# Performance work log

Hardware: AMD Instinct MI355X
Metric: run time of the kernel (lower is better)

Reference implementation:

```python
import jax, jax.numpy as jnp
import numpy as np

B, N = 2, 1024
DIM = 1024
DQK = 128
NUM_KEYS = 256
NUM_MEM = NUM_KEYS * NUM_KEYS
TOPK = 32
RANK = 2
HEADS = 2
DV = 512
KCONV = 5
MARGIN = 0.15
AUX_W = 0.1
MEM_LR = 10.0
RMS_EPS = 1.1920929e-07  # torch.finfo(float32).eps (RMSNorm eps=None default)
LN_EPS = 1e-5


def setup_inputs() -> dict:
    key = jax.random.key(0)
    ks = jax.random.split(key, 6)
    return {
        "tokens": jax.random.normal(ks[0], (B, N, DIM), jnp.float32),
        "rms_w": jnp.ones((DIM,), jnp.float32),
        "conv_w": jax.random.normal(ks[1], (DIM, 1, KCONV), jnp.float32) * 0.1,
        "conv_b": jnp.zeros((DIM,), jnp.float32),
        "wq": jax.random.normal(ks[2], (DQK, DIM), jnp.float32) * 0.02,
        "qln_w": jnp.ones((DQK,), jnp.float32),
        "keys": jax.random.normal(ks[3], (2, RANK, NUM_KEYS, DQK), jnp.float32) * 0.01,
        "core": jax.random.normal(ks[4], (HEADS, RANK, RANK), jnp.float32) * 0.01,
        "memories": jax.random.normal(ks[5], (NUM_MEM, DV), jnp.float32) * 0.01,
    }


def _forward(tokens, rms_w, conv_w, conv_b, wq, qln_w, keys, core, memories):
    # prenorm RMSNorm
    x = tokens * jax.lax.rsqrt(jnp.mean(tokens * tokens, -1, keepdims=True) + RMS_EPS) * rms_w
    # SVD of core; rank-1 merge vectors (first left/right singular vectors)
    u, s, vh = jnp.linalg.svd(core, full_matrices=False)
    u_vec = u[..., :, 0]   # (H, R)
    t_vec = vh[..., 0, :]  # (H, R)  == v[..., :, 0]
    aux = jnp.sum(jnp.mean(jnp.square(jax.nn.relu(s[:, 1:] - MARGIN)), -1)) * AUX_W
    # causal depthwise conv (left-pad KCONV-1)
    xc = jnp.swapaxes(x, 1, 2)  # (B, D, N)
    xc = jax.lax.conv_general_dilated(
        xc, conv_w, (1,), [(KCONV - 1, 0)],
        feature_group_count=DIM, dimension_numbers=('NCH', 'OIH', 'NCH'))
    x = jnp.swapaxes(xc + conv_b[None, :, None], 1, 2)
    # queries + LayerNorm (no bias). NOTE: original applies key_ln but then uses
    # the raw self.keys in the einsum, so key normalization is a no-op; replicated.
    q = x @ wq.T
    mu = jnp.mean(q, -1, keepdims=True)
    var = jnp.mean(jnp.square(q - mu), -1, keepdims=True)
    q = (q - mu) * jax.lax.rsqrt(var + LN_EPS) * qln_w
    # product-key scores: (2, B, N, M, R)
    sc = jnp.einsum('bnd,crmd->cbnmr', q, keys)
    row_sc, col_sc = sc[0], sc[1]  # (B, N, M, R)
    m_row = jnp.einsum('bnmr,hr->hbnm', row_sc, u_vec)
    m_col = jnp.einsum('bnmr,hr->hbnm', col_sc, t_vec)
    _, top_row = jax.lax.top_k(m_row, TOPK)  # (H, B, N, K)
    _, top_col = jax.lax.top_k(m_col, TOPK)
    # candidate flat memory indices: outer sum -> (H, B, N, K*K)
    idx = (top_row * NUM_KEYS)[..., :, None] + top_col[..., None, :]
    idx = idx.reshape(HEADS, B, N, TOPK * TOPK)
    # gather per-rank scores at the top row/col keys
    rs = jnp.broadcast_to(row_sc[None], (HEADS,) + row_sc.shape)
    cs = jnp.broadcast_to(col_sc[None], (HEADS,) + col_sc.shape)
    ri = jnp.broadcast_to(top_row[..., None], top_row.shape + (RANK,))
    ci = jnp.broadcast_to(top_col[..., None], top_col.shape + (RANK,))
    f_row = jnp.take_along_axis(rs, ri, axis=3)  # (H, B, N, K, R)
    f_col = jnp.take_along_axis(cs, ci, axis=3)
    # bilinear core combine over ranks -> (H, B, N, K, K)
    scores = jnp.einsum('hbnir,hbnjs,hrs->hbnij', f_row, f_col, core)
    scores = scores.reshape(HEADS, B, N, TOPK * TOPK)
    fs, top_m = jax.lax.top_k(scores, TOPK)
    f_idx = jnp.take_along_axis(idx, top_m, axis=-1)  # (H, B, N, K)
    fs = jax.nn.sigmoid(fs)
    # gather from memory table: (H, B, N, K, DV)
    mem = memories[f_idx]
    # scale_gradient exactly as written: detach(t) - s*t + detach(s*t)  (grad = -s)
    scaled = mem * MEM_LR
    mem = jax.lax.stop_gradient(mem) - scaled + jax.lax.stop_gradient(scaled)
    agg = jnp.einsum('hbnkd,hbnk->hbnd', mem, fs)
    out = jnp.transpose(agg, (1, 2, 0, 3)).reshape(B, N, HEADS * DV)
    # combine_values_to_out is Identity (heads * dim_values == dim)
    return out, aux


def reference(tokens, rms_w, conv_w, conv_b, wq, qln_w, keys, core, memories):
    return _forward(tokens, rms_w, conv_w, conv_b, wq, qln_w, keys, core, memories)
```

## Files before the change

kernel.cpp:

```cpp
#include <hip/hip_runtime.h>
#include <math.h>


#define ROWS 2048

__device__ inline double dsgn(double x, double y) { return (y >= 0.0) ? fabs(x) : -fabs(x); }

__device__ void dlasv2_dev(double f, double g, double h,
                           double& ssmin, double& ssmax,
                           double& snr, double& csr, double& snl, double& csl)
{
  const double EPSD = 2.2204460492503131e-16;
  double ft = f, fa = fabs(f), ht = h, ha = fabs(h);
  int pmax = 1;
  bool swp = (ha > fa);
  if (swp) { pmax = 3; double tp = ft; ft = ht; ht = tp; tp = fa; fa = ha; ha = tp; }
  double gt = g, ga = fabs(gt);
  double clt = 0.0, crt = 0.0, slt = 0.0, srt = 0.0;
  if (ga == 0.0) {
    ssmin = ha; ssmax = fa; clt = 1.0; crt = 1.0; slt = 0.0; srt = 0.0;
  } else {
    bool gasmal = true;
    if (ga > fa) {
      pmax = 2;
// ... 45 lines not shown
  for (int hh = 0; hh < 2; hh++) {
    double a = (double)core[hh * 4 + 0];
    double b = (double)core[hh * 4 + 1];
    double c = (double)core[hh * 4 + 2];
    double d = (double)core[hh * 4 + 3];
    double tau = 0.0, v2 = 0.0, d1, e, d2;
    if (c != 0.0) {
      double nrm  = sqrt(a * a + c * c);
      double beta = (a >= 0.0) ? -nrm : nrm;
      tau = (beta - a) / beta;
      v2  = c / (a - beta);
      double wsum = b + v2 * d;
      d1 = beta;
      e  = b - tau * wsum;
      d2 = d - tau * v2 * wsum;
    } else { d1 = a; e = b; d2 = d; }
    double ssmin, ssmax, snr, csr, snl, csl;
    dlasv2_dev(d1, e, d2, ssmin, ssmax, snr, csr, snl, csl);
    double t0 = csl + v2 * snl;
    double u0 = csl - tau * t0;
    double u1 = snl - tau * v2 * t0;
    double sg = (ssmax < 0.0) ? -1.0 : 1.0;
    misc[hh * 2 + 0]     = (float)u0;
    misc[hh * 2 + 1]     = (float)u1;
    misc[4 + hh * 2 + 0] = (float)(sg * csr);
    misc[4 + hh * 2 + 1] = (float)(sg * snr);
    double s2 = fabs(ssmin);
    double rl = s2 - 0.15; if (rl < 0.0) rl = 0.0;
    aux += rl * rl;
  }
  aux_out[0] = (float)(aux * 0.1);
}

__global__ __launch_bounds__(256) void conv_kernel(const float* __restrict__ tokens,
                                                   const float* __restrict__ rms_w,
                                                   const float* __restrict__ conv_w,
                                                   const float* __restrict__ conv_b,
                                                   const float* __restrict__ core,
                                                   float* __restrict__ misc,
                                                   float* __restrict__ aux_out,
                                                   float* __restrict__ x2)
{
  __shared__ float x_l[12][1024];
  __shared__ float red[12][4];
  __shared__ float inv_s[12];
  const int t    = threadIdx.x;
  const int row0 = blockIdx.x * 8;
  const int n0   = row0 & 1023;
  const int c0   = t * 4;

  float sq[12];
  #pragma unroll
  for (int s = 0; s < 12; s++) {
    float4 v = make_float4(0.f, 0.f, 0.f, 0.f);
    if (n0 - 4 + s >= 0)
      v = *(const float4*)(tokens + (size_t)(row0 - 4 + s) * 1024 + c0);
    *(float4*)&x_l[s][c0] = v;
    sq[s] = v.x * v.x + v.y * v.y + v.z * v.z + v.w * v.w;
  }
  #pragma unroll
  for (int off = 32; off; off >>= 1) {
    #pragma unroll
    for (int s = 0; s < 12; s++) sq[s] += __shfl_down(sq[s], off, 64);
  }
  const int lane = t & 63, wv_id = t >> 6;
  if (lane == 0) {
    #pragma unroll
    for (int s = 0; s < 12; s++) red[s][wv_id] = sq[s];
  }
  __syncthreads();
  if (t < 12)
    inv_s[t] = rsqrtf((red[t][0] + red[t][1] + red[t][2] + red[t][3]) * (1.0f / 1024.0f)
                      + 1.1920929e-07f);
  __syncthreads();
  #pragma unroll
  for (int s = 0; s < 12; s++) {
    float iv = inv_s[s];
    float4 v = *(float4*)&x_l[s][c0];
    v.x *= iv; v.y *= iv; v.z *= iv; v.w *= iv;
    *(float4*)&x_l[s][c0] = v;
  }
  float wv[20];
  const float* cw = conv_w + (size_t)c0 * 5;
  #pragma unroll
  for (int i = 0; i < 5; i++) {
    float4 u = *(const float4*)(cw + i * 4);
    wv[i * 4 + 0] = u.x; wv[i * 4 + 1] = u.y; wv[i * 4 + 2] = u.z; wv[i * 4 + 3] = u.w;
  }
  float4 rw = *(const float4*)(rms_w + c0);
  float4 cb = *(const float4*)(conv_b + c0);
  #pragma unroll
  for (int r = 0; r < 8; r++) {
    float4 acc = make_float4(0.f, 0.f, 0.f, 0.f);
    #pragma unroll
    for (int k = 0; k < 5; k++) {
      float4 x4 = *(const float4*)&x_l[r + k][c0];
      acc.x = fmaf(x4.x, wv[0 * 5 + k], acc.x);
      acc.y = fmaf(x4.y, wv[1 * 5 + k], acc.y);
      acc.z = fmaf(x4.z, wv[2 * 5 + k], acc.z);
      acc.w = fmaf(x4.w, wv[3 * 5 + k], acc.w);
    }
    acc.x = acc.x * rw.x + cb.x;
    acc.y = acc.y * rw.y + cb.y;
    acc.z = acc.z * rw.z + cb.z;
    acc.w = acc.w * rw.w + cb.w;
    *(float4*)(x2 + (size_t)(row0 + r) * 1024 + c0) = acc;
  }
  if (blockIdx.x == 0 && t == 0) do_svd(core, misc, aux_out);
}

__global__ __launch_bounds__(256) void gemm_kernel(const float* __restrict__ A, int lda,
                                                   const float* __restrict__ Bm, int ldb,
                                                   float* __restrict__ C, int ldc,
                                                   int koffy, int coffy, int poffy)
{
  __shared__ __align__(16) float a_lds[32 * 64];
  __shared__ __align__(16) float b_lds[32 * 128];
  const int t  = threadIdx.x;
  const int rb = blockIdx.x * 64;
  const int kb = blockIdx.y * koffy;
  const int cb = blockIdx.y * coffy;
  C += (size_t)blockIdx.y * (size_t)poffy;
  const int tx = t & 31, ty = t >> 5;
  const int c0 = tx * 4, r0 = ty * 8;
  float acc[8][4];
  #pragma unroll
  for (int i = 0; i < 8; i++)
    #pragma unroll
    for (int j = 0; j < 4; j++) acc[i][j] = 0.0f;

  const int ra = t & 63,  kqa = (t >> 6) * 8;
  const int ob = t >> 1,  kqb = (t & 1) * 16;

  for (int kt = 0; kt < 4; kt++) {
    const int k0 = kb + kt * 32;
    {
      const float* ap = A + (size_t)(rb + ra) * lda + k0 + kqa;
      float4 a0 = *(const float4*)(ap);
      float4 a1 = *(const float4*)(ap + 4);
      a_lds[(kqa + 0) * 64 + ra] = a0.x;
      a_lds[(kqa + 1) * 64 + ra] = a0.y;
      a_lds[(kqa + 2) * 64 + ra] = a0.z;
      a_lds[(kqa + 3) * 64 + ra] = a0.w;
      a_lds[(kqa + 4) * 64 + ra] = a1.x;
      a_lds[(kqa + 5) * 64 + ra] = a1.y;
      a_lds[(kqa + 6) * 64 + ra] = a1.z;
      a_lds[(kqa + 7) * 64 + ra] = a1.w;
    }
    {
      const float* bp = Bm + (size_t)(cb + ob) * ldb + k0 + kqb;
      float4 b0 = *(const float4*)(bp);
      float4 b1 = *(const float4*)(bp + 4);
      float4 b2 = *(const float4*)(bp + 8);
      float4 b3 = *(const float4*)(bp + 12);
      b_lds[(kqb +  0) * 128 + ob] = b0.x;
      b_lds[(kqb +  1) * 128 + ob] = b0.y;
      b_lds[(kqb +  2) * 128 + ob] = b0.z;
      b_lds[(kqb +  3) * 128 + ob] = b0.w;
      b_lds[(kqb +  4) * 128 + ob] = b1.x;
      b_lds[(kqb +  5) * 128 + ob] = b1.y;
      b_lds[(kqb +  6) * 128 + ob] = b1.z;
      b_lds[(kqb +  7) * 128 + ob] = b1.w;
      b_lds[(kqb +  8) * 128 + ob] = b2.x;
      b_lds[(kqb +  9) * 128 + ob] = b2.y;
      b_lds[(kqb + 10) * 128 + ob] = b2.z;
      b_lds[(kqb + 11) * 128 + ob] = b2.w;
      b_lds[(kqb + 12) * 128 + ob] = b3.x;
      b_lds[(kqb + 13) * 128 + ob] = b3.y;
      b_lds[(kqb + 14) * 128 + ob] = b3.z;
      b_lds[(kqb + 15) * 128 + ob] = b3.w;
    }
    __syncthreads();
    #pragma unroll
    for (int k = 0; k < 32; k++) {
      float4 av0 = *(const float4*)(a_lds + k * 64 + r0);
      float4 av1 = *(const float4*)(a_lds + k * 64 + r0 + 4);
      float4 bv  = *(const float4*)(b_lds + k * 128 + c0);
      float ar[8] = {av0.x, av0.y, av0.z, av0.w, av1.x, av1.y, av1.z, av1.w};
      float br[4] = {bv.x, bv.y, bv.z, bv.w};
      #pragma unroll
      for (int i = 0; i < 8; i++)
        #pragma unroll
        for (int j = 0; j < 4; j++)
          acc[i][j] = fmaf(ar[i], br[j], acc[i][j]);
    }
    __syncthreads();
  }
  #pragma unroll
  for (int i = 0; i < 8; i++) {
    float4 o4; o4.x = acc[i][0]; o4.y = acc[i][1]; o4.z = acc[i][2]; o4.w = acc[i][3];
    *(float4*)(C + (size_t)(rb + r0 + i) * ldc + cb + c0) = o4;
  }
}

__global__ __launch_bounds__(256) void gemm2ln_kernel(const float* __restrict__ qpart,
                                                      const float* __restrict__ qln_w,
                                                      const float* __restrict__ keys,
                                                      float* __restrict__ C)
{
  __shared__ __align__(16) float a_l[128 * 64];
  __shared__ __align__(16) float b_lds[32 * 128];
  const int t  = threadIdx.x;
  const int rb = blockIdx.x * 64;
  const int cb = blockIdx.y * 128;

  const int l32 = t & 31;
  const int g32 = t >> 5;
  float vs[8][4];
  #pragma unroll
  for (int j = 0; j < 8; j++) { vs[j][0]=0.f; vs[j][1]=0.f; vs[j][2]=0.f; vs[j][3]=0.f; }
  #pragma unroll
  for (int g = 0; g < 8; g++) {
    const float* pg = qpart + (size_t)g * (ROWS * 128) + (size_t)rb * 128 + l32 * 4;
    #pragma unroll
    for (int j = 0; j < 8; j++) {
      float4 v = *(const float4*)(pg + (g32 + 8 * j) * 128);
      vs[j][0] += v.x; vs[j][1] += v.y; vs[j][2] += v.z; vs[j][3] += v.w;
    }
  }
  float4 qw = *(const float4*)(qln_w + l32 * 4);
  #pragma unroll
  for (int j = 0; j < 8; j++) {
    float s1 = vs[j][0] + vs[j][1] + vs[j][2] + vs[j][3];
    #pragma unroll
    for (int off = 16; off; off >>= 1) s1 += __shfl_xor(s1, off, 32);
    float mu = s1 * (1.0f / 128.0f);
    float d0 = vs[j][0] - mu, d1 = vs[j][1] - mu, d2 = vs[j][2] - mu, d3 = vs[j][3] - mu;
    float s2 = d0 * d0 + d1 * d1 + d2 * d2 + d3 * d3;
    #pragma unroll
    for (int off = 16; off; off >>= 1) s2 += __shfl_xor(s2, off, 32);
    float rstd = rsqrtf(s2 * (1.0f / 128.0f) + 1e-5f);
    const int row = g32 + 8 * j;
    a_l[(l32 * 4 + 0) * 64 + row] = d0 * rstd * qw.x;
    a_l[(l32 * 4 + 1) * 64 + row] = d1 * rstd * qw.y;
    a_l[(l32 * 4 + 2) * 64 + row] = d2 * rstd * qw.z;
    a_l[(l32 * 4 + 3) * 64 + row] = d3 * rstd * qw.w;
  }
  __syncthreads();

  const int tx = t & 31, ty = t >> 5;
  const int c0 = tx * 4, r0 = ty * 8;
  float acc[8][4];
  #pragma unroll
  for (int i = 0; i < 8; i++)
    #pragma unroll
    for (int j = 0; j < 4; j++) acc[i][j] = 0.0f;

  const int ob = t >> 1, kqb = (t & 1) * 16;
  for (int kt = 0; kt < 4; kt++) {
    const int k0 = kt * 32;
    {
      const float* bp = keys + (size_t)(cb + ob) * 128 + k0 + kqb;
      float4 b0 = *(const float4*)(bp);
      float4 b1 = *(const float4*)(bp + 4);
      float4 b2 = *(const float4*)(bp + 8);
      float4 b3 = *(const float4*)(bp + 12);
      b_lds[(kqb +  0) * 128 + ob] = b0.x;
      b_lds[(kqb +  1) * 128 + ob] = b0.y;
      b_lds[(kqb +  2) * 128 + ob] = b0.z;
      b_lds[(kqb +  3) * 128 + ob] = b0.w;
      b_lds[(kqb +  4) * 128 + ob] = b1.x;
      b_lds[(kqb +  5) * 128 + ob] = b1.y;
      b_lds[(kqb +  6) * 128 + ob] = b1.z;
      b_lds[(kqb +  7) * 128 + ob] = b1.w;
      b_lds[(kqb +  8) * 128 + ob] = b2.x;
      b_lds[(kqb +  9) * 128 + ob] = b2.y;
      b_lds[(kqb + 10) * 128 + ob] = b2.z;
      b_lds[(kqb + 11) * 128 + ob] = b2.w;
      b_lds[(kqb + 12) * 128 + ob] = b3.x;
      b_lds[(kqb + 13) * 128 + ob] = b3.y;
      b_lds[(kqb + 14) * 128 + ob] = b3.z;
      b_lds[(kqb + 15) * 128 + ob] = b3.w;
    }
    __syncthreads();
    #pragma unroll
    for (int k = 0; k < 32; k++) {
      float4 av0 = *(const float4*)(a_l + (k0 + k) * 64 + r0);
      float4 av1 = *(const float4*)(a_l + (k0 + k) * 64 + r0 + 4);
      float4 bv  = *(const float4*)(b_lds + k * 128 + c0);
      float ar[8] = {av0.x, av0.y, av0.z, av0.w, av1.x, av1.y, av1.z, av1.w};
      float br[4] = {bv.x, bv.y, bv.z, bv.w};
      #pragma unroll
      for (int i = 0; i < 8; i++)
        #pragma unroll
        for (int j = 0; j < 4; j++)
          acc[i][j] = fmaf(ar[i], br[j], acc[i][j]);
    }
    __syncthreads();
  }
  #pragma unroll
  for (int i = 0; i < 8; i++) {
    float4 o4; o4.x = acc[i][0]; o4.y = acc[i][1]; o4.z = acc[i][2]; o4.w = acc[i][3];
    *(float4*)(C + (size_t)(rb + r0 + i) * 1024 + cb + c0) = o4;
  }
}

__device__ inline unsigned f2ord(float f) {
  unsigned u = __float_as_uint(f);
  return (u & 0x80000000u) ? ~u : (u | 0x80000000u);
}
__device__ inline int lpc(unsigned long long m) {
  return __builtin_amdgcn_mbcnt_hi((unsigned)(m >> 32),
         __builtin_amdgcn_mbcnt_lo((unsigned)m, 0));
}

__global__ __launch_bounds__(256) void tail_kernel(const float* __restrict__ sc,
                                                   const float* __restrict__ misc,
                                                   const float* __restrict__ core,
                                                   const float* __restrict__ memories,
                                                   float* __restrict__ out)
{
  __shared__ __align__(16) float s_pl[1024];
  __shared__ int   tkbuf[4][32];
  __shared__ float mvals[4][32];
  __shared__ int   mcand[4][32];
  __shared__ int   s_idx[64];
  __shared__ float s_w[64];

  const int row = blockIdx.x;
  const int tid = threadIdx.x;
  ((float4*)s_pl)[tid] = ((const float4*)(sc + (size_t)row * 1024))[tid];
  __syncthreads();

  const int w = tid >> 6, lane = tid & 63;

  {
    const int h = w >> 1, side = w & 1;
    const float v0 = misc[side * 4 + h * 2 + 0];
    const float v1 = misc[side * 4 + h * 2 + 1];
    const float* p0 = s_pl + side * 512;
    const float* p1 = p0 + 256;
    const int mb = lane * 4;
    float4 a4 = *(const float4*)(p0 + mb);
    float4 b4 = *(const float4*)(p1 + mb);
    unsigned kk[4];
    kk[0] = f2ord(a4.x * v0 + b4.x * v1);
    kk[1] = f2ord(a4.y * v0 + b4.y * v1);
    kk[2] = f2ord(a4.z * v0 + b4.z * v1);
    kk[3] = f2ord(a4.w * v0 + b4.w * v1);
    unsigned tau = 0u;
    #pragma unroll
    for (int b = 31; b >= 0; --b) {
      unsigned cand = tau | (1u << b);
      int cnt = 0;
      #pragma unroll
      for (int i = 0; i < 4; i++) cnt += __popcll(__ballot(kk[i] >= cand));
      if (cnt >= 32) tau = cand;
    }
    unsigned long long bG[4], bE[4];
    int cntG = 0, sbG = 0, sbE = 0;
    #pragma unroll
    for (int i = 0; i < 4; i++) {
      bG[i] = __ballot(kk[i] > tau);
      bE[i] = __ballot(kk[i] == tau);
      cntG += __popcll(bG[i]);
      sbG  += lpc(bG[i]);
      sbE  += lpc(bE[i]);
    }
    const int need = 32 - cntG;
    int runG = 0, runE = 0;
    #pragma unroll
    for (int i = 0; i < 4; i++) {
      if (kk[i] > tau)       { tkbuf[w][sbG + runG] = mb + i; runG++; }
      else if (kk[i] == tau) {
        int r = sbE + runE;
        if (r < need) tkbuf[w][cntG + r] = mb + i;
        runE++;
      }
    }
  }
  __syncthreads();

  {
    const int h = w >> 1, half = w & 1;
    const float c00 = core[h * 4 + 0], c01 = core[h * 4 + 1];
    const float c10 = core[h * 4 + 2], c11 = core[h * 4 + 3];
    const int i_glob = half * 16 + (lane >> 2);
    const int ri = tkbuf[h * 2 + 0][i_glob];
    const float fr0 = s_pl[ri], fr1 = s_pl[256 + ri];
    const float a0 = fr0 * c00 + fr1 * c10;
    const float a1 = fr0 * c01 + fr1 * c11;
    const int j0 = (lane & 3) * 8;
    float sv[8];
    unsigned kk[8];
    #pragma unroll
    for (int t2 = 0; t2 < 8; t2++) {
      int cj = tkbuf[h * 2 + 1][j0 + t2];
      sv[t2] = a0 * s_pl[512 + cj] + a1 * s_pl[768 + cj];
      kk[t2] = f2ord(sv[t2]);
    }
    unsigned tau = 0u;
    #pragma unroll
    for (int b = 31; b >= 0; --b) {
      unsigned cand = tau | (1u << b);
      int cnt = 0;
      #pragma unroll
      for (int i = 0; i < 8; i++) cnt += __popcll(__ballot(kk[i] >= cand));
      if (cnt >= 32) tau = cand;
    }
    unsigned long long bG[8], bE[8];
    int cntG = 0, sbG = 0, sbE = 0;
    #pragma unroll
    for (int i = 0; i < 8; i++) {
      bG[i] = __ballot(kk[i] > tau);
      bE[i] = __ballot(kk[i] == tau);
      cntG += __popcll(bG[i]);
      sbG  += lpc(bG[i]);
      sbE  += lpc(bE[i]);
    }
    const int need = 32 - cntG;
    int runG = 0, runE = 0;
    #pragma unroll
    for (int i = 0; i < 8; i++) {
      int c = i_glob * 32 + j0 + i;
      if (kk[i] > tau) {
        mvals[w][sbG + runG] = sv[i]; mcand[w][sbG + runG] = c; runG++;
      } else if (kk[i] == tau) {
        int r = sbE + runE;
        if (r < need) { mvals[w][cntG + r] = sv[i]; mcand[w][cntG + r] = c; }
        runE++;
      }
    }
  }
  __syncthreads();

  if (w < 2) {
    const int h = w;
    const int half2 = lane >> 5, k = lane & 31;
    const float v = mvals[h * 2 + half2][k];
    const int   c = mcand[h * 2 + half2][k];
    int cnt = 0;
    #pragma unroll 8
    for (int j = 0; j < 64; j++) {
      float u = mvals[h * 2 + (j >> 5)][j & 31];
      int  uc = mcand[h * 2 + (j >> 5)][j & 31];
      cnt += (u > v || (u == v && uc < c)) ? 1 : 0;
    }
    if (cnt < 32) {
      int ii = c >> 5, jj = c & 31;
      s_idx[h * 32 + cnt] = tkbuf[h * 2][ii] * 256 + tkbuf[h * 2 + 1][jj];
      s_w[h * 32 + cnt]   = 1.0f / (1.0f + expf(-v));
    }
  }
  __syncthreads();

  const int h2 = tid >> 7;
  const int d4 = tid & 127;
  const int base = h2 * 32;
  const float* mb = memories + d4 * 4;
  float ax = 0.f, ay = 0.f, az = 0.f, aw = 0.f;
  float4 va[8], vb[8];
  float  wa[8], wb[8];
  #pragma unroll
  for (int i = 0; i < 8; i++) {
    int mi = s_idx[base + i]; wa[i] = s_w[base + i];
    va[i] = *(const float4*)(mb + (size_t)mi * 512);
  }
  #pragma unroll
  for (int i = 0; i < 8; i++) {
    int mi = s_idx[base + 8 + i]; wb[i] = s_w[base + 8 + i];
    vb[i] = *(const float4*)(mb + (size_t)mi * 512);
  }
  #pragma unroll
  for (int i = 0; i < 8; i++) {
    ax = fmaf(wa[i], va[i].x, ax); ay = fmaf(wa[i], va[i].y, ay);
    az = fmaf(wa[i], va[i].z, az); aw = fmaf(wa[i], va[i].w, aw);
  }
  #pragma unroll
  for (int i = 0; i < 8; i++) {
    int mi = s_idx[base + 16 + i]; wa[i] = s_w[base + 16 + i];
    va[i] = *(const float4*)(mb + (size_t)mi * 512);
  }
  #pragma unroll
  for (int i = 0; i < 8; i++) {
    ax = fmaf(wb[i], vb[i].x, ax); ay = fmaf(wb[i], vb[i].y, ay);
    az = fmaf(wb[i], vb[i].z, az); aw = fmaf(wb[i], vb[i].w, aw);
  }
  #pragma unroll
  for (int i = 0; i < 8; i++) {
    int mi = s_idx[base + 24 + i]; wb[i] = s_w[base + 24 + i];
    vb[i] = *(const float4*)(mb + (size_t)mi * 512);
  }
  #pragma unroll
  for (int i = 0; i < 8; i++) {
    ax = fmaf(wa[i], va[i].x, ax); ay = fmaf(wa[i], va[i].y, ay);
    az = fmaf(wa[i], va[i].z, az); aw = fmaf(wa[i], va[i].w, aw);
  }
  #pragma unroll
  for (int i = 0; i < 8; i++) {
    ax = fmaf(wb[i], vb[i].x, ax); ay = fmaf(wb[i], vb[i].y, ay);
    az = fmaf(wb[i], vb[i].z, az); aw = fmaf(wb[i], vb[i].w, aw);
  }
  float4 o4; o4.x = ax; o4.y = ay; o4.z = az; o4.w = aw;
  ((float4*)out)[(size_t)row * 256 + tid] = o4;
}

extern "C" void kernel_launch(void* const* d_in, const int* in_sizes, int n_in,
                              void* d_out, int out_size, void* d_ws, size_t ws_size,
                              hipStream_t stream) {
  const float* tokens = (const float*)d_in[0];
  const float* rms_w  = (const float*)d_in[1];
  const float* conv_w = (const float*)d_in[2];
  const float* conv_b = (const float*)d_in[3];
  const float* wq     = (const float*)d_in[4];
  const float* qln_w  = (const float*)d_in[5];
  const float* keys   = (const float*)d_in[6];
  const float* core   = (const float*)d_in[7];
  const float* mems   = (const float*)d_in[8];
  float* out = (float*)d_out;
  float* ws  = (float*)d_ws;

  float* misc   = ws;
  float* x2     = ws + 4096;
  float* qpart  = x2 + 2097152;
  float* sc     = x2;

  conv_kernel  <<<ROWS / 8, 256, 0, stream>>>(tokens, rms_w, conv_w, conv_b,
                                              core, misc, out + 2097152, x2);
  gemm_kernel  <<<dim3(32, 8), 256, 0, stream>>>(x2, 1024, wq, 1024,
                                                 qpart, 128, 128, 0, ROWS * 128);
  gemm2ln_kernel<<<dim3(32, 8), 256, 0, stream>>>(qpart, qln_w, keys, sc);
  tail_kernel  <<<ROWS, 256, 0, stream>>>(sc, misc, core, mems, out);
}
```

Before: 278.3 us.

## Fuse norm, conv, query GEMM, key scoring and memory gather into one kernel

Replaces the four-kernel pipeline (conv, split-K query GEMM, LayerNorm plus key GEMM, tail top-k and gather) with a single kernel where each block handles 4 rows end to end in shared memory. This removes the intermediate global buffers for x2, partial q and scores, plus three launch boundaries. In exchange, every block rereads the full wq matrix (128x1024) and keys for only 4 rows, the GEMMs run as scalar FMAs with little register reuse, and each block redundantly recomputes the core SVD on one thread. Only 512 blocks are launched.

Result: slower. 324.1 us (+16.5%).

```diff
diff --git a/kernel.cpp b/kernel.cpp
--- a/kernel.cpp
+++ b/kernel.cpp
@@ -101,269 +101,6 @@
   aux_out[0] = (float)(aux * 0.1);
 }
 
-__global__ __launch_bounds__(256) void conv_kernel(const float* __restrict__ tokens,
-                                                   const float* __restrict__ rms_w,
-                                                   const float* __restrict__ conv_w,
-                                                   const float* __restrict__ conv_b,
-                                                   const float* __restrict__ core,
-                                                   float* __restrict__ misc,
-                                                   float* __restrict__ aux_out,
-                                                   float* __restrict__ x2)
-{
-  __shared__ float x_l[12][1024];
-  __shared__ float red[12][4];
-  __shared__ float inv_s[12];
-  const int t    = threadIdx.x;
-  const int row0 = blockIdx.x * 8;
-  const int n0   = row0 & 1023;
-  const int c0   = t * 4;
-
-  float sq[12];
-  #pragma unroll
-  for (int s = 0; s < 12; s++) {
-    float4 v = make_float4(0.f, 0.f, 0.f, 0.f);
-    if (n0 - 4 + s >= 0)
-      v = *(const float4*)(tokens + (size_t)(row0 - 4 + s) * 1024 + c0);
-    *(float4*)&x_l[s][c0] = v;
-    sq[s] = v.x * v.x + v.y * v.y + v.z * v.z + v.w * v.w;
-  }
-  #pragma unroll
-  for (int off = 32; off; off >>= 1) {
-    #pragma unroll
-    for (int s = 0; s < 12; s++) sq[s] += __shfl_down(sq[s], off, 64);
-  }
-  const int lane = t & 63, wv_id = t >> 6;
-  if (lane == 0) {
-    #pragma unroll
-    for (int s = 0; s < 12; s++) red[s][wv_id] = sq[s];
-  }
-  __syncthreads();
-  if (t < 12)
-    inv_s[t] = rsqrtf((red[t][0] + red[t][1] + red[t][2] + red[t][3]) * (1.0f / 1024.0f)
-                      + 1.1920929e-07f);
-  __syncthreads();
-  #pragma unroll
-  for (int s = 0; s < 12; s++) {
-    float iv = inv_s[s];
-    float4 v = *(float4*)&x_l[s][c0];
-    v.x *= iv; v.y *= iv; v.z *= iv; v.w *= iv;
-    *(float4*)&x_l[s][c0] = v;
-  }
-  float wv[20];
-  const float* cw = conv_w + (size_t)c0 * 5;
-  #pragma unroll
-  for (int i = 0; i < 5; i++) {
-    float4 u = *(const float4*)(cw + i * 4);
-    wv[i * 4 + 0] = u.x; wv[i * 4 + 1] = u.y; wv[i * 4 + 2] = u.z; wv[i * 4 + 3] = u.w;
-  }
-  float4 rw = *(const float4*)(rms_w + c0);
-  float4 cb = *(const float4*)(conv_b + c0);
-  #pragma unroll
-  for (int r = 0; r < 8; r++) {
-    float4 acc = make_float4(0.f, 0.f, 0.f, 0.f);
-    #pragma unroll
-    for (int k = 0; k < 5; k++) {
-      float4 x4 = *(const float4*)&x_l[r + k][c0];
-      acc.x = fmaf(x4.x, wv[0 * 5 + k], acc.x);
-      acc.y = fmaf(x4.y, wv[1 * 5 + k], acc.y);
-      acc.z = fmaf(x4.z, wv[2 * 5 + k], acc.z);
-      acc.w = fmaf(x4.w, wv[3 * 5 + k], acc.w);
-    }
-    acc.x = acc.x * rw.x + cb.x;
-    acc.y = acc.y * rw.y + cb.y;
-    acc.z = acc.z * rw.z + cb.z;
-    acc.w = acc.w * rw.w + cb.w;
-    *(float4*)(x2 + (size_t)(row0 + r) * 1024 + c0) = acc;
-  }
-  if (blockIdx.x == 0 && t == 0) do_svd(core, misc, aux_out);
-}
-
-__global__ __launch_bounds__(256) void gemm_kernel(const float* __restrict__ A, int lda,
-                                                   const float* __restrict__ Bm, int ldb,
-                                                   float* __restrict__ C, int ldc,
-                                                   int koffy, int coffy, int poffy)
-{
-  __shared__ __align__(16) float a_lds[32 * 64];
-  __shared__ __align__(16) float b_lds[32 * 128];
-  const int t  = threadIdx.x;
-  const int rb = blockIdx.x * 64;
-  const int kb = blockIdx.y * koffy;
-  const int cb = blockIdx.y * coffy;
-  C += (size_t)blockIdx.y * (size_t)poffy;
-  const int tx = t & 31, ty = t >> 5;
-  const int c0 = tx * 4, r0 = ty * 8;
-  float acc[8][4];
-  #pragma unroll
-  for (int i = 0; i < 8; i++)
-    #pragma unroll
-    for (int j = 0; j < 4; j++) acc[i][j] = 0.0f;
-
-  const int ra = t & 63,  kqa = (t >> 6) * 8;
-  const int ob = t >> 1,  kqb = (t & 1) * 16;
-
-  for (int kt = 0; kt < 4; kt++) {
-    const int k0 = kb + kt * 32;
-    {
-      const float* ap = A + (size_t)(rb + ra) * lda + k0 + kqa;
-      float4 a0 = *(const float4*)(ap);
-      float4 a1 = *(const float4*)(ap + 4);
-      a_lds[(kqa + 0) * 64 + ra] = a0.x;
-      a_lds[(kqa + 1) * 64 + ra] = a0.y;
-      a_lds[(kqa + 2) * 64 + ra] = a0.z;
-      a_lds[(kqa + 3) * 64 + ra] = a0.w;
-      a_lds[(kqa + 4) * 64 + ra] = a1.x;
-      a_lds[(kqa + 5) * 64 + ra] = a1.y;
-      a_lds[(kqa + 6) * 64 + ra] = a1.z;
-      a_lds[(kqa + 7) * 64 + ra] = a1.w;
-    }
-    {
-      const float* bp = Bm + (size_t)(cb + ob) * ldb + k0 + kqb;
-      float4 b0 = *(const float4*)(bp);
-      float4 b1 = *(const float4*)(bp + 4);
-      float4 b2 = *(const float4*)(bp + 8);
-      float4 b3 = *(const float4*)(bp + 12);
-      b_lds[(kqb +  0) * 128 + ob] = b0.x;
-      b_lds[(kqb +  1) * 128 + ob] = b0.y;
-      b_lds[(kqb +  2) * 128 + ob] = b0.z;
-      b_lds[(kqb +  3) * 128 + ob] = b0.w;
-      b_lds[(kqb +  4) * 128 + ob] = b1.x;
-      b_lds[(kqb +  5) * 128 + ob] = b1.y;
-      b_lds[(kqb +  6) * 128 + ob] = b1.z;
-      b_lds[(kqb +  7) * 128 + ob] = b1.w;
-      b_lds[(kqb +  8) * 128 + ob] = b2.x;
-      b_lds[(kqb +  9) * 128 + ob] = b2.y;
-      b_lds[(kqb + 10) * 128 + ob] = b2.z;
-      b_lds[(kqb + 11) * 128 + ob] = b2.w;
-      b_lds[(kqb + 12) * 128 + ob] = b3.x;
-      b_lds[(kqb + 13) * 128 + ob] = b3.y;
-      b_lds[(kqb + 14) * 128 + ob] = b3.z;
-      b_lds[(kqb + 15) * 128 + ob] = b3.w;
-    }
-    __syncthreads();
-    #pragma unroll
-    for (int k = 0; k < 32; k++) {
-      float4 av0 = *(const float4*)(a_lds + k * 64 + r0);
-      float4 av1 = *(const float4*)(a_lds + k * 64 + r0 + 4);
-      float4 bv  = *(const float4*)(b_lds + k * 128 + c0);
-      float ar[8] = {av0.x, av0.y, av0.z, av0.w, av1.x, av1.y, av1.z, av1.w};
-      float br[4] = {bv.x, bv.y, bv.z, bv.w};
-      #pragma unroll
-      for (int i = 0; i < 8; i++)
-        #pragma unroll
-        for (int j = 0; j < 4; j++)
-          acc[i][j] = fmaf(ar[i], br[j], acc[i][j]);
-    }
-    __syncthreads();
-  }
-  #pragma unroll
-  for (int i = 0; i < 8; i++) {
-    float4 o4; o4.x = acc[i][0]; o4.y = acc[i][1]; o4.z = acc[i][2]; o4.w = acc[i][3];
-    *(float4*)(C + (size_t)(rb + r0 + i) * ldc + cb + c0) = o4;
-  }
-}
-
-__global__ __launch_bounds__(256) void gemm2ln_kernel(const float* __restrict__ qpart,
-                                                      const float* __restrict__ qln_w,
-                                                      const float* __restrict__ keys,
-                                                      float* __restrict__ C)
-{
-  __shared__ __align__(16) float a_l[128 * 64];
-  __shared__ __align__(16) float b_lds[32 * 128];
-  const int t  = threadIdx.x;
-  const int rb = blockIdx.x * 64;
-  const int cb = blockIdx.y * 128;
-
-  const int l32 = t & 31;
-  const int g32 = t >> 5;
-  float vs[8][4];
-  #pragma unroll
-  for (int j = 0; j < 8; j++) { vs[j][0]=0.f; vs[j][1]=0.f; vs[j][2]=0.f; vs[j][3]=0.f; }
-  #pragma unroll
-  for (int g = 0; g < 8; g++) {
-    const float* pg = qpart + (size_t)g * (ROWS * 128) + (size_t)rb * 128 + l32 * 4;
-    #pragma unroll
-    for (int j = 0; j < 8; j++) {
-      float4 v = *(const float4*)(pg + (g32 + 8 * j) * 128);
-      vs[j][0] += v.x; vs[j][1] += v.y; vs[j][2] += v.z; vs[j][3] += v.w;
-    }
-  }
-  float4 qw = *(const float4*)(qln_w + l32 * 4);
-  #pragma unroll
-  for (int j = 0; j < 8; j++) {
-    float s1 = vs[j][0] + vs[j][1] + vs[j][2] + vs[j][3];
-    #pragma unroll
-    for (int off = 16; off; off >>= 1) s1 += __shfl_xor(s1, off, 32);
-    float mu = s1 * (1.0f / 128.0f);
-    float d0 = vs[j][0] - mu, d1 = vs[j][1] - mu, d2 = vs[j][2] - mu, d3 = vs[j][3] - mu;
-    float s2 = d0 * d0 + d1 * d1 + d2 * d2 + d3 * d3;
-    #pragma unroll
-    for (int off = 16; off; off >>= 1) s2 += __shfl_xor(s2, off, 32);
-    float rstd = rsqrtf(s2 * (1.0f / 128.0f) + 1e-5f);
-    const int row = g32 + 8 * j;
-    a_l[(l32 * 4 + 0) * 64 + row] = d0 * rstd * qw.x;
-    a_l[(l32 * 4 + 1) * 64 + row] = d1 * rstd * qw.y;
-    a_l[(l32 * 4 + 2) * 64 + row] = d2 * rstd * qw.z;
-    a_l[(l32 * 4 + 3) * 64 + row] = d3 * rstd * qw.w;
-  }
-  __syncthreads();
-
-  const int tx = t & 31, ty = t >> 5;
-  const int c0 = tx * 4, r0 = ty * 8;
-  float acc[8][4];
-  #pragma unroll
-  for (int i = 0; i < 8; i++)
-    #pragma unroll
-    for (int j = 0; j < 4; j++) acc[i][j] = 0.0f;
-
-  const int ob = t >> 1, kqb = (t & 1) * 16;
-  for (int kt = 0; kt < 4; kt++) {
-    const int k0 = kt * 32;
-    {
-      const float* bp = keys + (size_t)(cb + ob) * 128 + k0 + kqb;
-      float4 b0 = *(const float4*)(bp);
-      float4 b1 = *(const float4*)(bp + 4);
-      float4 b2 = *(const float4*)(bp + 8);
-      float4 b3 = *(const float4*)(bp + 12);
-      b_lds[(kqb +  0) * 128 + ob] = b0.x;
-      b_lds[(kqb +  1) * 128 + ob] = b0.y;
-      b_lds[(kqb +  2) * 128 + ob] = b0.z;
-      b_lds[(kqb +  3) * 128 + ob] = b0.w;
-      b_lds[(kqb +  4) * 128 + ob] = b1.x;
-      b_lds[(kqb +  5) * 128 + ob] = b1.y;
-      b_lds[(kqb +  6) * 128 + ob] = b1.z;
-      b_lds[(kqb +  7) * 128 + ob] = b1.w;
-      b_lds[(kqb +  8) * 128 + ob] = b2.x;
-      b_lds[(kqb +  9) * 128 + ob] = b2.y;
-      b_lds[(kqb + 10) * 128 + ob] = b2.z;
-      b_lds[(kqb + 11) * 128 + ob] = b2.w;
-      b_lds[(kqb + 12) * 128 + ob] = b3.x;
-      b_lds[(kqb + 13) * 128 + ob] = b3.y;
-      b_lds[(kqb + 14) * 128 + ob] = b3.z;
-      b_lds[(kqb + 15) * 128 + ob] = b3.w;
-    }
-    __syncthreads();
-    #pragma unroll
-    for (int k = 0; k < 32; k++) {
-      float4 av0 = *(const float4*)(a_l + (k0 + k) * 64 + r0);
-      float4 av1 = *(const float4*)(a_l + (k0 + k) * 64 + r0 + 4);
-      float4 bv  = *(const float4*)(b_lds + k * 128 + c0);
-      float ar[8] = {av0.x, av0.y, av0.z, av0.w, av1.x, av1.y, av1.z, av1.w};
-      float br[4] = {bv.x, bv.y, bv.z, bv.w};
-      #pragma unroll
-      for (int i = 0; i < 8; i++)
-        #pragma unroll
-        for (int j = 0; j < 4; j++)
-          acc[i][j] = fmaf(ar[i], br[j], acc[i][j]);
-    }
-    __syncthreads();
-  }
-  #pragma unroll
-  for (int i = 0; i < 8; i++) {
-    float4 o4; o4.x = acc[i][0]; o4.y = acc[i][1]; o4.z = acc[i][2]; o4.w = acc[i][3];
-    *(float4*)(C + (size_t)(rb + r0 + i) * 1024 + cb + c0) = o4;
-  }
-}
-
 __device__ inline unsigned f2ord(float f) {
   unsigned u = __float_as_uint(f);
   return (u & 0x80000000u) ? ~u : (u | 0x80000000u);
@@ -373,195 +110,383 @@
          __builtin_amdgcn_mbcnt_lo((unsigned)m, 0));
 }
 
-__global__ __launch_bounds__(256) void tail_kernel(const float* __restrict__ sc,
-                                                   const float* __restrict__ misc,
-                                                   const float* __restrict__ core,
-                                                   const float* __restrict__ memories,
-                                                   float* __restrict__ out)
+__global__ __launch_bounds__(256) void fused_kernel(
+    const float* __restrict__ tokens, const float* __restrict__ rms_w,
+    const float* __restrict__ conv_w, const float* __restrict__ conv_b,
+    const float* __restrict__ wq,     const float* __restrict__ qln_w,
+    const float* __restrict__ keys,   const float* __restrict__ core,
+    const float* __restrict__ memories,
+    float* __restrict__ out)
 {
-  __shared__ __align__(16) float s_pl[1024];
-  __shared__ int   tkbuf[4][32];
-  __shared__ float mvals[4][32];
-  __shared__ int   mcand[4][32];
-  __shared__ int   s_idx[64];
-  __shared__ float s_w[64];
-
-  const int row = blockIdx.x;
-  const int tid = threadIdx.x;
-  ((float4*)s_pl)[tid] = ((const float4*)(sc + (size_t)row * 1024))[tid];
+  __shared__ __align__(16) float smem[13400];
+  float* x_l    = smem;
+  float* sc_l   = smem + 4096;
+  float* b_l    = smem + 8192;
+  float* qbuf   = smem + 12288;
+  float* redp   = smem + 12800;
+  float* invp   = smem + 12832;
+  float* misc_l = smem + 12840;
+  float* aux_l  = smem + 12848;
+  int*   tkbuf  = (int*)(smem + 12852);
+  float* mvals  = smem + 12980;
+  int*   mcand  = (int*)(smem + 13108);
+  int*   s_idx  = (int*)(smem + 13236);
+  float* s_w    = smem + 13300;
+
+  const int bid  = blockIdx.x;
+  const int t    = threadIdx.x;
+  const int row0 = bid * 4;
+  const int n0   = row0 & 1023;
+  const int c0   = t * 4;
+  const int lane = t & 63, w = t >> 6;
+
+  {
+    float sq[8];
+    #pragma unroll
+    for (int s = 0; s < 8; s++) {
+      float4 v = make_float4(0.f, 0.f, 0.f, 0.f);
+      if (n0 - 4 + s >= 0)
+        v = *(const float4*)(tokens + (size_t)(row0 - 4 + s) * 1024 + c0);
+      *(float4*)&x_l[s * 1024 + c0] = v;
+      sq[s] = v.x * v.x + v.y * v.y + v.z * v.z + v.w * v.w;
+    }
+    #pragma unroll
+    for (int off = 32; off; off >>= 1) {
+      #pragma unroll
+      for (int s = 0; s < 8; s++) sq[s] += __shfl_down(sq[s], off, 64);
+    }
+    if (lane == 0) {
+      #pragma unroll
+      for (int s = 0; s < 8; s++) redp[s * 4 + w] = sq[s];
+    }
+    __syncthreads();
+    if (t < 8)
+      invp[t] = rsqrtf((redp[t * 4 + 0] + redp[t * 4 + 1] + redp[t * 4 + 2] + redp[t * 4 + 3])
+                       * (1.0f / 1024.0f) + 1.1920929e-07f);
+    if (t == 0) do_svd(core, misc_l, aux_l);
+    __syncthreads();
+    #pragma unroll
+    for (int s = 0; s < 8; s++) {
+      float iv = invp[s];
+      float4 v = *(float4*)&x_l[s * 1024 + c0];
+      v.x *= iv; v.y *= iv; v.z *= iv; v.w *= iv;
+      *(float4*)&x_l[s * 1024 + c0] = v;
+    }
+    float wv[20];
+    const float* cw = conv_w + (size_t)c0 * 5;
+    #pragma unroll
+    for (int i = 0; i < 5; i++) {
+      float4 u = *(const float4*)(cw + i * 4);
+      wv[i * 4 + 0] = u.x; wv[i * 4 + 1] = u.y; wv[i * 4 + 2] = u.z; wv[i * 4 + 3] = u.w;
+    }
+    float4 rw = *(const float4*)(rms_w + c0);
+    float4 cb = *(const float4*)(conv_b + c0);
+    #pragma unroll
+    for (int r = 0; r < 4; r++) {
+      float4 acc = make_float4(0.f, 0.f, 0.f, 0.f);
+      #pragma unroll
+      for (int k = 0; k < 5; k++) {
+        float4 x4 = *(const float4*)&x_l[(r + k) * 1024 + c0];
+        acc.x = fmaf(x4.x, wv[0 * 5 + k], acc.x);
+        acc.y = fmaf(x4.y, wv[1 * 5 + k], acc.y);
+        acc.z = fmaf(x4.z, wv[2 * 5 + k], acc.z);
+        acc.w = fmaf(x4.w, wv[3 * 5 + k], acc.w);
+      }
+      acc.x = acc.x * rw.x + cb.x;
+      acc.y = acc.y * rw.y + cb.y;
+      acc.z = acc.z * rw.z + cb.z;
+      acc.w = acc.w * rw.w + cb.w;
+      *(float4*)&x_l[r * 1024 + c0] = acc;
+    }
+    if (bid == 0 && t == 0) out[2097152] = aux_l[0];
+  }
   __syncthreads();
 
-  const int w = tid >> 6, lane = tid & 63;
-
   {
-    const int h = w >> 1, side = w & 1;
-    const float v0 = misc[side * 4 + h * 2 + 0];
-    const float v1 = misc[side * 4 + h * 2 + 1];
-    const float* p0 = s_pl + side * 512;
-    const float* p1 = p0 + 256;
-    const int mb = lane * 4;
-    float4 a4 = *(const float4*)(p0 + mb);
-    float4 b4 = *(const float4*)(p1 + mb);
-    unsigned kk[4];
-    kk[0] = f2ord(a4.x * v0 + b4.x * v1);
-    kk[1] = f2ord(a4.y * v0 + b4.y * v1);
-    kk[2] = f2ord(a4.z * v0 + b4.z * v1);
-    kk[3] = f2ord(a4.w * v0 + b4.w * v1);
-    unsigned tau = 0u;
-    #pragma unroll
-    for (int b = 31; b >= 0; --b) {
-      unsigned cand = tau | (1u << b);
+    const int col = t & 127, tp = t >> 7;
+    const int ob = t >> 1, kq = (t & 1) * 16;
+    float a0 = 0.f, a1 = 0.f;
+    for (int kt = 0; kt < 32; kt++) {
+      const int k0 = kt * 32;
+      {
+        const float* bp = wq + (size_t)ob * 1024 + k0 + kq;
+        float4 b0 = *(const float4*)(bp);
+        float4 b1 = *(const float4*)(bp + 4);
+        float4 b2 = *(const float4*)(bp + 8);
+        float4 b3 = *(const float4*)(bp + 12);
+        b_l[(kq +  0) * 128 + ob] = b0.x;  b_l[(kq +  1) * 128 + ob] = b0.y;
+        b_l[(kq +  2) * 128 + ob] = b0.z;  b_l[(kq +  3) * 128 + ob] = b0.w;
+        b_l[(kq +  4) * 128 + ob] = b1.x;  b_l[(kq +  5) * 128 + ob] = b1.y;
+        b_l[(kq +  6) * 128 + ob] = b1.z;  b_l[(kq +  7) * 128 + ob] = b1.w;
+        b_l[(kq +  8) * 128 + ob] = b2.x;  b_l[(kq +  9) * 128 + ob] = b2.y;
+        b_l[(kq + 10) * 128 + ob] = b2.z;  b_l[(kq + 11) * 128 + ob] = b2.w;
+        b_l[(kq + 12) * 128 + ob] = b3.x;  b_l[(kq + 13) * 128 + ob] = b3.y;
+        b_l[(kq + 14) * 128 + ob] = b3.z;  b_l[(kq + 15) * 128 + ob] = b3.w;
+      }
+      __syncthreads();
+      const float* xA = x_l + (size_t)(tp * 2) * 1024 + k0;
+      const float* xB = xA + 1024;
+      #pragma unroll
+      for (int kk = 0; kk < 32; kk += 4) {
+        float4 a4 = *(const float4*)(xA + kk);
+        float4 b4 = *(const float4*)(xB + kk);
+        float w0 = b_l[(kk + 0) * 128 + col];
+        float w1 = b_l[(kk + 1) * 128 + col];
+        float w2 = b_l[(kk + 2) * 128 + col];
+        float w3 = b_l[(kk + 3) * 128 + col];
+        a0 = fmaf(a4.x, w0, a0); a0 = fmaf(a4.y, w1, a0);
+        a0 = fmaf(a4.z, w2, a0); a0 = fmaf(a4.w, w3, a0);
+        a1 = fmaf(b4.x, w0, a1); a1 = fmaf(b4.y, w1, a1);
+        a1 = fmaf(b4.z, w2, a1); a1 = fmaf(b4.w, w3, a1);
+      }
+      __syncthreads();
+    }
+    qbuf[(tp * 2 + 0) * 128 + col] = a0;
+    qbuf[(tp * 2 + 1) * 128 + col] = a1;
+  }
+  __syncthreads();
+
+  {
+    float v0 = qbuf[w * 128 + lane];
+    float v1 = qbuf[w * 128 + lane + 64];
+    float s1 = v0 + v1;
+    #pragma unroll
+    for (int off = 32; off; off >>= 1) s1 += __shfl_xor(s1, off, 64);
+    float mu = s1 * (1.0f / 128.0f);
+    float d0 = v0 - mu, d1 = v1 - mu;
+    float s2 = d0 * d0 + d1 * d1;
+    #pragma unroll
+    for (int off = 32; off; off >>= 1) s2 += __shfl_xor(s2, off, 64);
+    float rstd = rsqrtf(s2 * (1.0f / 128.0f) + 1e-5f);
+    qbuf[w * 128 + lane]      = d0 * rstd * qln_w[lane];
+    qbuf[w * 128 + lane + 64] = d1 * rstd * qln_w[lane + 64];
+  }
+  __syncthreads();
+
+  {
+    const int col = t & 127, tp = t >> 7;
+    const int ob = t >> 1, kq = (t & 1) * 16;
+    for (int ct = 0; ct < 8; ct++) {
+      const int cb = ct * 128;
+      float a0 = 0.f, a1 = 0.f;
+      for (int kt = 0; kt < 4; kt++) {
+        const int k0 = kt * 32;
+        {
+          const float* bp = keys + (size_t)(cb + ob) * 128 + k0 + kq;
+          float4 b0 = *(const float4*)(bp);
+          float4 b1 = *(const float4*)(bp + 4);
+          float4 b2 = *(const float4*)(bp + 8);
+          float4 b3 = *(const float4*)(bp + 12);
+          b_l[(kq +  0) * 128 + ob] = b0.x;  b_l[(kq +  1) * 128 + ob] = b0.y;
+          b_l[(kq +  2) * 128 + ob] = b0.z;  b_l[(kq +  3) * 128 + ob] = b0.w;
+          b_l[(kq +  4) * 128 + ob] = b1.x;  b_l[(kq +  5) * 128 + ob] = b1.y;
+          b_l[(kq +  6) * 128 + ob] = b1.z;  b_l[(kq +  7) * 128 + ob] = b1.w;
+          b_l[(kq +  8) * 128 + ob] = b2.x;  b_l[(kq +  9) * 128 + ob] = b2.y;
+          b_l[(kq + 10) * 128 + ob] = b2.z;  b_l[(kq + 11) * 128 + ob] = b2.w;
+          b_l[(kq + 12) * 128 + ob] = b3.x;  b_l[(kq + 13) * 128 + ob] = b3.y;
+          b_l[(kq + 14) * 128 + ob] = b3.z;  b_l[(kq + 15) * 128 + ob] = b3.w;
+        }
+        __syncthreads();
+        const float* qA = qbuf + (size_t)(tp * 2) * 128 + k0;
+        const float* qB = qA + 128;
+        #pragma unroll
+        for (int kk = 0; kk < 32; kk += 4) {
+          float4 a4 = *(const float4*)(qA + kk);
+          float4 b4 = *(const float4*)(qB + kk);
+          float w0 = b_l[(kk + 0) * 128 + col];
+          float w1 = b_l[(kk + 1) * 128 + col];
+          float w2 = b_l[(kk + 2) * 128 + col];
+          float w3 = b_l[(kk + 3) * 128 + col];
+          a0 = fmaf(a4.x, w0, a0); a0 = fmaf(a4.y, w1, a0);
+          a0 = fmaf(a4.z, w2, a0); a0 = fmaf(a4.w, w3, a0);
+          a1 = fmaf(b4.x, w0, a1); a1 = fmaf(b4.y, w1, a1);
+          a1 = fmaf(b4.z, w2, a1); a1 = fmaf(b4.w, w3, a1);
+        }
+        __syncthreads();
+      }
+      sc_l[(tp * 2 + 0) * 1024 + cb + col] = a0;
+      sc_l[(tp * 2 + 1) * 1024 + cb + col] = a1;
+    }
+  }
+
+  const int h2 = t >> 7;
+  const int d4 = t & 127;
+  const int gbase = h2 * 32;
+  const float* mp = memories + d4 * 4;
+
+  for (int rr = 0; rr < 4; rr++) {
+    __syncthreads();
+    const int row = row0 + rr;
+    const float* s_pl = sc_l + rr * 1024;
+
+    {
+      const int h = w >> 1, side = w & 1;
+      const float v0 = misc_l[side * 4 + h * 2 + 0];
+      const float v1 = misc_l[side * 4 + h * 2 + 1];
+      const float* p0 = s_pl + side * 512;
+      const float* p1 = p0 + 256;
+      const int mb = lane * 4;
+      float4 a4 = *(const float4*)(p0 + mb);
+      float4 b4 = *(const float4*)(p1 + mb);
+      unsigned kk[4];
+      kk[0] = f2ord(a4.x * v0 + b4.x * v1);
+      kk[1] = f2ord(a4.y * v0 + b4.y * v1);
+      kk[2] = f2ord(a4.z * v0 + b4.z * v1);
+      kk[3] = f2ord(a4.w * v0 + b4.w * v1);
+      unsigned tau = 0u;
+      #pragma unroll
+      for (int b = 31; b >= 0; --b) {
+        unsigned cand = tau | (1u << b);
+        int cnt = 0;
+        #pragma unroll
+        for (int i = 0; i < 4; i++) cnt += __popcll(__ballot(kk[i] >= cand));
+        if (cnt >= 32) tau = cand;
+      }
+      unsigned long long bG[4], bE[4];
+      int cntG = 0, sbG = 0, sbE = 0;
+      #pragma unroll
+      for (int i = 0; i < 4; i++) {
+        bG[i] = __ballot(kk[i] > tau);
+        bE[i] = __ballot(kk[i] == tau);
+        cntG += __popcll(bG[i]);
+        sbG  += lpc(bG[i]);
+        sbE  += lpc(bE[i]);
+      }
+      const int need = 32 - cntG;
+      int runG = 0, runE = 0;
+      #pragma unroll
+      for (int i = 0; i < 4; i++) {
+        if (kk[i] > tau)       { tkbuf[w * 32 + sbG + runG] = mb + i; runG++; }
+        else if (kk[i] == tau) {
+          int r = sbE + runE;
+          if (r < need) tkbuf[w * 32 + cntG + r] = mb + i;
+          runE++;
+        }
+      }
+    }
+    __syncthreads();
+
+    {
+      const int h = w >> 1, half = w & 1;
+      const float c00 = core[h * 4 + 0], c01 = core[h * 4 + 1];
+      const float c10 = core[h * 4 + 2], c11 = core[h * 4 + 3];
+      const int i_glob = half * 16 + (lane >> 2);
+      const int ri = tkbuf[(h * 2 + 0) * 32 + i_glob];
+      const float fr0 = s_pl[ri], fr1 = s_pl[256 + ri];
+      const float a0 = fr0 * c00 + fr1 * c10;
+      const float a1 = fr0 * c01 + fr1 * c11;
+      const int j0 = (lane & 3) * 8;
+      float sv[8];
+      unsigned kk[8];
+      #pragma unroll
+      for (int t2 = 0; t2 < 8; t2++) {
+        int cj = tkbuf[(h * 2 + 1) * 32 + j0 + t2];
+        sv[t2] = a0 * s_pl[512 + cj] + a1 * s_pl[768 + cj];
+        kk[t2] = f2ord(sv[t2]);
+      }
+      unsigned tau = 0u;
+      #pragma unroll
+      for (int b = 31; b >= 0; --b) {
+        unsigned cand = tau | (1u << b);
+        int cnt = 0;
+        #pragma unroll
+        for (int i = 0; i < 8; i++) cnt += __popcll(__ballot(kk[i] >= cand));
+        if (cnt >= 32) tau = cand;
+      }
+      unsigned long long bG[8], bE[8];
+      int cntG = 0, sbG = 0, sbE = 0;
+      #pragma unroll
+      for (int i = 0; i < 8; i++) {
+        bG[i] = __ballot(kk[i] > tau);
+        bE[i] = __ballot(kk[i] == tau);
+        cntG += __popcll(bG[i]);
+        sbG  += lpc(bG[i]);
+        sbE  += lpc(bE[i]);
+      }
+      const int need = 32 - cntG;
+      int runG = 0, runE = 0;
+      #pragma unroll
+      for (int i = 0; i < 8; i++) {
+        int c = i_glob * 32 + j0 + i;
+        if (kk[i] > tau) {
+          mvals[w * 32 + sbG + runG] = sv[i]; mcand[w * 32 + sbG + runG] = c; runG++;
+        } else if (kk[i] == tau) {
+          int r = sbE + runE;
+          if (r < need) { mvals[w * 32 + cntG + r] = sv[i]; mcand[w * 32 + cntG + r] = c; }
+          runE++;
+        }
+      }
+    }
+    __syncthreads();
+
+    if (w < 2) {
+      const int h = w;
+      const int half2 = lane >> 5, k = lane & 31;
+      const float v = mvals[(h * 2 + half2) * 32 + k];
+      const int   c = mcand[(h * 2 + half2) * 32 + k];
       int cnt = 0;
-      #pragma unroll
-      for (int i = 0; i < 4; i++) cnt += __popcll(__ballot(kk[i] >= cand));
-      if (cnt >= 32) tau = cand;
-    }
-    unsigned long long bG[4], bE[4];
-    int cntG = 0, sbG = 0, sbE = 0;
-    #pragma unroll
-    for (int i = 0; i < 4; i++) {
-      bG[i] = __ballot(kk[i] > tau);
-      bE[i] = __ballot(kk[i] == tau);
-      cntG += __popcll(bG[i]);
-      sbG  += lpc(bG[i]);
-      sbE  += lpc(bE[i]);
-    }
-    const int need = 32 - cntG;
-    int runG = 0, runE = 0;
-    #pragma unroll
-    for (int i = 0; i < 4; i++) {
-      if (kk[i] > tau)       { tkbuf[w][sbG + runG] = mb + i; runG++; }
-      else if (kk[i] == tau) {
-        int r = sbE + runE;
-        if (r < need) tkbuf[w][cntG + r] = mb + i;
-        runE++;
-      }
-    }
-  }
-  __syncthreads();
-
-  {
-    const int h = w >> 1, half = w & 1;
-    const float c00 = core[h * 4 + 0], c01 = core[h * 4 + 1];
-    const float c10 = core[h * 4 + 2], c11 = core[h * 4 + 3];
-    const int i_glob = half * 16 + (lane >> 2);
-    const int ri = tkbuf[h * 2 + 0][i_glob];
-    const float fr0 = s_pl[ri], fr1 = s_pl[256 + ri];
-    const float a0 = fr0 * c00 + fr1 * c10;
-    const float a1 = fr0 * c01 + fr1 * c11;
-    const int j0 = (lane & 3) * 8;
-    float sv[8];
-    unsigned kk[8];
-    #pragma unroll
-    for (int t2 = 0; t2 < 8; t2++) {
-      int cj = tkbuf[h * 2 + 1][j0 + t2];
-      sv[t2] = a0 * s_pl[512 + cj] + a1 * s_pl[768 + cj];
-      kk[t2] = f2ord(sv[t2]);
-    }
-    unsigned tau = 0u;
-    #pragma unroll
-    for (int b = 31; b >= 0; --b) {
-      unsigned cand = tau | (1u << b);
-      int cnt = 0;
-      #pragma unroll
-      for (int i = 0; i < 8; i++) cnt += __popcll(__ballot(kk[i] >= cand));
-      if (cnt >= 32) tau = cand;
-    }
-    unsigned long long bG[8], bE[8];
-    int cntG = 0, sbG = 0, sbE = 0;
-    #pragma unroll
-    for (int i = 0; i < 8; i++) {
-      bG[i] = __ballot(kk[i] > tau);
-      bE[i] = __ballot(kk[i] == tau);
-      cntG += __popcll(bG[i]);
-      sbG  += lpc(bG[i]);
-      sbE  += lpc(bE[i]);
-    }
-    const int need = 32 - cntG;
-    int runG = 0, runE = 0;
-    #pragma unroll
-    for (int i = 0; i < 8; i++) {
-      int c = i_glob * 32 + j0 + i;
-      if (kk[i] > tau) {
-        mvals[w][sbG + runG] = sv[i]; mcand[w][sbG + runG] = c; runG++;
-      } else if (kk[i] == tau) {
-        int r = sbE + runE;
-        if (r < need) { mvals[w][cntG + r] = sv[i]; mcand[w][cntG + r] = c; }
-        runE++;
-      }
-    }
-  }
-  __syncthreads();
-
-  if (w < 2) {
-    const int h = w;
-    const int half2 = lane >> 5, k = lane & 31;
-    const float v = mvals[h * 2 + half2][k];
-    const int   c = mcand[h * 2 + half2][k];
-    int cnt = 0;
-    #pragma unroll 8
-    for (int j = 0; j < 64; j++) {
-      float u = mvals[h * 2 + (j >> 5)][j & 31];
-      int  uc = mcand[h * 2 + (j >> 5)][j & 31];
-      cnt += (u > v || (u == v && uc < c)) ? 1 : 0;
-    }
-    if (cnt < 32) {
-      int ii = c >> 5, jj = c & 31;
-      s_idx[h * 32 + cnt] = tkbuf[h * 2][ii] * 256 + tkbuf[h * 2 + 1][jj];
-      s_w[h * 32 + cnt]   = 1.0f / (1.0f + expf(-v));
-    }
-  }
-  __syncthreads();
-
-  const int h2 = tid >> 7;
-  const int d4 = tid & 127;
-  const int base = h2 * 32;
-  const float* mb = memories + d4 * 4;
-  float ax = 0.f, ay = 0.f, az = 0.f, aw = 0.f;
-  float4 va[8], vb[8];
-  float  wa[8], wb[8];
-  #pragma unroll
-  for (int i = 0; i < 8; i++) {
-    int mi = s_idx[base + i]; wa[i] = s_w[base + i];
-    va[i] = *(const float4*)(mb + (size_t)mi * 512);
-  }
-  #pragma unroll
-  for (int i = 0; i < 8; i++) {
-    int mi = s_idx[base + 8 + i]; wb[i] = s_w[base + 8 + i];
-    vb[i] = *(const float4*)(mb + (size_t)mi * 512);
-  }
-  #pragma unroll
-  for (int i = 0; i < 8; i++) {
-    ax = fmaf(wa[i], va[i].x, ax); ay = fmaf(wa[i], va[i].y, ay);
-    az = fmaf(wa[i], va[i].z, az); aw = fmaf(wa[i], va[i].w, aw);
-  }
-  #pragma unroll
-  for (int i = 0; i < 8; i++) {
-    int mi = s_idx[base + 16 + i]; wa[i] = s_w[base + 16 + i];
-    va[i] = *(const float4*)(mb + (size_t)mi * 512);
-  }
-  #pragma unroll
-  for (int i = 0; i < 8; i++) {
-    ax = fmaf(wb[i], vb[i].x, ax); ay = fmaf(wb[i], vb[i].y, ay);
-    az = fmaf(wb[i], vb[i].z, az); aw = fmaf(wb[i], vb[i].w, aw);
-  }
-  #pragma unroll
-  for (int i = 0; i < 8; i++) {
-    int mi = s_idx[base + 24 + i]; wb[i] = s_w[base + 24 + i];
-    vb[i] = *(const float4*)(mb + (size_t)mi * 512);
-  }
-  #pragma unroll
-  for (int i = 0; i < 8; i++) {
-    ax = fmaf(wa[i], va[i].x, ax); ay = fmaf(wa[i], va[i].y, ay);
-    az = fmaf(wa[i], va[i].z, az); aw = fmaf(wa[i], va[i].w, aw);
-  }
-  #pragma unroll
-  for (int i = 0; i < 8; i++) {
-    ax = fmaf(wb[i], vb[i].x, ax); ay = fmaf(wb[i], vb[i].y, ay);
-    az = fmaf(wb[i], vb[i].z, az); aw = fmaf(wb[i], vb[i].w, aw);
-  }
-  float4 o4; o4.x = ax; o4.y = ay; o4.z = az; o4.w = aw;
-  ((float4*)out)[(size_t)row * 256 + tid] = o4;
+      #pragma unroll 8
+      for (int j = 0; j < 64; j++) {
+        float u = mvals[(h * 2 + (j >> 5)) * 32 + (j & 31)];
+        int  uc = mcand[(h * 2 + (j >> 5)) * 32 + (j & 31)];
+        cnt += (u > v || (u == v && uc < c)) ? 1 : 0;
+      }
+      if (cnt < 32) {
+        int ii = c >> 5, jj = c & 31;
+        s_idx[h * 32 + cnt] = tkbuf[(h * 2) * 32 + ii] * 256 + tkbuf[(h * 2 + 1) * 32 + jj];
+        s_w[h * 32 + cnt]   = 1.0f / (1.0f + expf(-v));
+      }
+    }
+    __syncthreads();
+
+    {
+      float ax = 0.f, ay = 0.f, az = 0.f, aw = 0.f;
+      float4 va[8], vb[8];
+      float  wa[8], wb[8];
+      #pragma unroll
+      for (int i = 0; i < 8; i++) {
+        int mi = s_idx[gbase + i]; wa[i] = s_w[gbase + i];
+        va[i] = *(const float4*)(mp + (size_t)mi * 512);
+      }
+      #pragma unroll
+      for (int i = 0; i < 8; i++) {
+        int mi = s_idx[gbase + 8 + i]; wb[i] = s_w[gbase + 8 + i];
+        vb[i] = *(const float4*)(mp + (size_t)mi * 512);
+      }
+      #pragma unroll
+      for (int i = 0; i < 8; i++) {
+        ax = fmaf(wa[i], va[i].x, ax); ay = fmaf(wa[i], va[i].y, ay);
+        az = fmaf(wa[i], va[i].z, az); aw = fmaf(wa[i], va[i].w, aw);
+      }
+      #pragma unroll
+      for (int i = 0; i < 8; i++) {
+        int mi = s_idx[gbase + 16 + i]; wa[i] = s_w[gbase + 16 + i];
+        va[i] = *(const float4*)(mp + (size_t)mi * 512);
+      }
+      #pragma unroll
+      for (int i = 0; i < 8; i++) {
+        ax = fmaf(wb[i], vb[i].x, ax); ay = fmaf(wb[i], vb[i].y, ay);
+        az = fmaf(wb[i], vb[i].z, az); aw = fmaf(wb[i], vb[i].w, aw);
+      }
+      #pragma unroll
+      for (int i = 0; i < 8; i++) {
+        int mi = s_idx[gbase + 24 + i]; wb[i] = s_w[gbase + 24 + i];
+        vb[i] = *(const float4*)(mp + (size_t)mi * 512);
+      }
+      #pragma unroll
+      for (int i = 0; i < 8; i++) {
+        ax = fmaf(wa[i], va[i].x, ax); ay = fmaf(wa[i], va[i].y, ay);
+        az = fmaf(wa[i], va[i].z, az); aw = fmaf(wa[i], va[i].w, aw);
+      }
+      #pragma unroll
+      for (int i = 0; i < 8; i++) {
+        ax = fmaf(wb[i], vb[i].x, ax); ay = fmaf(wb[i], vb[i].y, ay);
+        az = fmaf(wb[i], vb[i].z, az); aw = fmaf(wb[i], vb[i].w, aw);
+      }
+      float4 o4; o4.x = ax; o4.y = ay; o4.z = az; o4.w = aw;
+      ((float4*)out)[(size_t)row * 256 + t] = o4;
+    }
+  }
 }
 
 extern "C" void kernel_launch(void* const* d_in, const int* in_sizes, int n_in,
@@ -577,17 +502,8 @@
   const float* core   = (const float*)d_in[7];
   const float* mems   = (const float*)d_in[8];
   float* out = (float*)d_out;
-  float* ws  = (float*)d_ws;
-
-  float* misc   = ws;
-  float* x2     = ws + 4096;
-  float* qpart  = x2 + 2097152;
-  float* sc     = x2;
-
-  conv_kernel  <<<ROWS / 8, 256, 0, stream>>>(tokens, rms_w, conv_w, conv_b,
-                                              core, misc, out + 2097152, x2);
-  gemm_kernel  <<<dim3(32, 8), 256, 0, stream>>>(x2, 1024, wq, 1024,
-                                                 qpart, 128, 128, 0, ROWS * 128);
-  gemm2ln_kernel<<<dim3(32, 8), 256, 0, stream>>>(qpart, qln_w, keys, sc);
-  tail_kernel  <<<ROWS, 256, 0, stream>>>(sc, misc, core, mems, out);
+  (void)d_ws; (void)ws_size;
+
+  fused_kernel<<<ROWS / 4, 256, 0, stream>>>(tokens, rms_w, conv_w, conv_b,
+                                             wq, qln_w, keys, core, mems, out);
 }
```
